# Performance work log

Hardware: AMD Instinct MI355X
Metric: run time of the kernel (lower is better)

## Reference

```python
import jax, jax.numpy as jnp
import numpy as np

NUM_CLASSES = 81
BACKGROUND = 0
TOP_K = 200
KEEP_TOP_K = 200
CONF_THR = 0.01
NMS_THR = 0.45
B = 32
P = 24564  # SSD512 prior count


def setup_inputs() -> dict:
    key = jax.random.key(0)
    k1, k2, kc, ks = jax.random.split(key, 4)
    loc_data = jax.random.normal(k1, (B, P * 4), jnp.float32) * 0.5
    conf_data = jax.random.uniform(k2, (B, P * NUM_CLASSES), dtype=jnp.float32)
    # priors in corner form [xmin,ymin,xmax,ymax] within [0,1], plus Caffe-style variances
    ctr = jax.random.uniform(kc, (P, 2), minval=0.05, maxval=0.95, dtype=jnp.float32)
    sz = jax.random.uniform(ks, (P, 2), minval=0.02, maxval=0.30, dtype=jnp.float32)
    pboxes = jnp.concatenate([ctr - sz * 0.5, ctr + sz * 0.5], axis=1)  # [P,4]
    variances = jnp.tile(jnp.array([0.1, 0.1, 0.2, 0.2], jnp.float32), (P, 1))  # [P,4]
    prior_data = jnp.stack([pboxes, variances], axis=0).reshape(1, 2, P * 4)
    return {"loc_data": loc_data, "conf_data": conf_data, "prior_data": prior_data}


def _decode(loc, priors, variances):
    # CENTER_SIZE decode, Caffe DetectionOutput convention (priors in corner form).
    pw = priors[:, 2] - priors[:, 0]
    ph = priors[:, 3] - priors[:, 1]
    pcx = (priors[:, 0] + priors[:, 2]) * 0.5
    pcy = (priors[:, 1] + priors[:, 3]) * 0.5
    cx = variances[:, 0] * loc[:, 0] * pw + pcx
    cy = variances[:, 1] * loc[:, 1] * ph + pcy
    w = jnp.exp(variances[:, 2] * loc[:, 2]) * pw
    h = jnp.exp(variances[:, 3] * loc[:, 3]) * ph
    return jnp.stack([cx - w * 0.5, cy - h * 0.5, cx + w * 0.5, cy + h * 0.5], axis=-1)


def _pairwise_iou(b):  # [K,4] -> [K,K]
    x1 = jnp.maximum(b[:, None, 0], b[None, :, 0])
    y1 = jnp.maximum(b[:, None, 1], b[None, :, 1])
    x2 = jnp.minimum(b[:, None, 2], b[None, :, 2])
    y2 = jnp.minimum(b[:, None, 3], b[None, :, 3])
    inter = jnp.clip(x2 - x1, 0.0) * jnp.clip(y2 - y1, 0.0)
    area = jnp.clip(b[:, 2] - b[:, 0], 0.0) * jnp.clip(b[:, 3] - b[:, 1], 0.0)
    union = area[:, None] + area[None, :] - inter
    return inter / jnp.maximum(union, 1e-10)


def _nms_one_class(scores, boxes):
    # scores: [P], boxes: [P,4] -> kept scores [TOP_K], candidate boxes [TOP_K,4]
    s = jnp.where(scores > CONF_THR, scores, -1.0)
    vals, idx = jax.lax.top_k(s, TOP_K)
    cand = boxes[idx]                      # [TOP_K,4]
    iou = _pairwise_iou(cand)              # [TOP_K,TOP_K]
    valid = vals > CONF_THR

    def body(i, carry):
        keep, suppressed = carry
        is_kept = valid[i] & jnp.logical_not(suppressed[i])
        keep = keep.at[i].set(is_kept)
        suppressed = suppressed | (is_kept & (iou[i] > NMS_THR))
        return keep, suppressed

    keep, _ = jax.lax.fori_loop(
        0, TOP_K, body,
        (jnp.zeros((TOP_K,), jnp.bool_), jnp.zeros((TOP_K,), jnp.bool_)))
    kept_scores = jnp.where(keep, vals, 0.0)
    return kept_scores, cand


def _detection_output(loc_data, conf_data, prior_data):
    bsz = loc_data.shape[0]
    nprior = loc_data.shape[1] // 4
    loc = loc_data.reshape(bsz, nprior, 4)
    conf = conf_data.reshape(bsz, nprior, NUM_CLASSES).transpose(0, 2, 1)  # [B,C,P]
    pr = prior_data.reshape(2, nprior, 4)
    priors, variances = pr[0], pr[1]

    decoded = jax.vmap(lambda l: _decode(l, priors, variances))(loc)  # [B,P,4]

    # kill background class
    bg = (jnp.arange(NUM_CLASSES) == BACKGROUND)[None, :, None]
    conf = jnp.where(bg, -1.0, conf)

    nms_bc = jax.vmap(jax.vmap(_nms_one_class, in_axes=(0, None)), in_axes=(0, 0))
    scores, cboxes = nms_bc(conf, decoded)  # [B,C,TOP_K], [B,C,TOP_K,4]

    flat_s = scores.reshape(bsz, NUM_CLASSES * TOP_K)
    top_s, top_i = jax.lax.top_k(flat_s, KEEP_TOP_K)          # [B,KEEP]
    labels = (top_i // TOP_K).astype(jnp.float32)
    flat_b = cboxes.reshape(bsz, NUM_CLASSES * TOP_K, 4)
    top_b = jnp.take_along_axis(flat_b, top_i[..., None], axis=1)  # [B,KEEP,4]

    img_id = jnp.broadcast_to(
        jnp.arange(bsz, dtype=jnp.float32)[:, None], (bsz, KEEP_TOP_K))
    rows = jnp.concatenate(
        [img_id[..., None], labels[..., None], top_s[..., None], top_b], axis=-1)
    rows = jnp.where((top_s > 0.0)[..., None], rows, 0.0)
    return rows[:, None, :, :]  # [B,1,KEEP_TOP_K,7]


def reference(loc_data, conf_data, prior_data):
    return _detection_output(loc_data, conf_data, prior_data)
```

## Files before the change

kernel.cpp:

```cpp
#include <hip/hip_runtime.h>
#include <stdint.h>

typedef uint32_t u32;
typedef uint64_t u64;
typedef uint16_t u16;

#define NCLS 81
#define TOPK 200
#define KEEPK 200
#define CONF_THR 0.01f
#define NMS_THR 0.45f
#define NB 32
#define NP 24564
#define NFLAT (NCLS * TOPK)
#define NPCHUNK 256
#define NCHUNK ((NP + NPCHUNK - 1) / NPCHUNK)
#define CAP 512
#define NBC (NB * NCLS)
#define LCAP 16
#define THRF 0.98828125f

__device__ __forceinline__ u32 fkey(float f) {
  u32 u = __float_as_uint(f);
  return (u & 0x80000000u) ? ~u : (u | 0x80000000u);
}
__device__ __forceinline__ float unfkey(u32 k) {
  u32 u = (k & 0x80000000u) ? (k & 0x7FFFFFFFu) : ~k;
  return __uint_as_float(u);
}

__global__ __launch_bounds__(256) void collect_cands(const float* __restrict__ conf,
                                                     u32* __restrict__ lcnt,
                                                     u64* __restrict__ lcand) {
  __shared__ u32 cnt81[NCLS];
  __shared__ u64 stage[NCLS * LCAP];

  const int tid = threadIdx.x;
  const int blk = blockIdx.x;
  const int b = blk / NCHUNK, chunk = blk % NCHUNK;
  const int p0 = chunk * NPCHUNK;
  const int cntp = min(NPCHUNK, NP - p0);
  const int tot4 = (cntp * NCLS) >> 2;
  const float4* __restrict__ src = (const float4*)(conf + ((size_t)b * NP + p0) * NCLS);

  for (int i = tid; i < NCLS; i += 256) cnt81[i] = 0u;
  __syncthreads();

  auto push = [&](int f, float s) {
    u32 pi = (u32)f / (u32)NCLS;
    u32 c = (u32)f - pi * (u32)NCLS;
    if (c != 0u) {
      u32 sl = atomicAdd(&cnt81[c], 1u);
      if (sl < (u32)LCAP) {
        u32 p = (u32)p0 + pi;
        stage[c * LCAP + sl] = ((u64)fkey(s) << 32) | (u32)(~p);
      }
    }
  };
  auto proc = [&](float4 v, int i4) {
    if (v.x >= THRF) push(i4 * 4 + 0, v.x);
    if (v.y >= THRF) push(i4 * 4 + 1, v.y);
    if (v.z >= THRF) push(i4 * 4 + 2, v.z);
    if (v.w >= THRF) push(i4 * 4 + 3, v.w);
  };

  for (int i = tid; i < tot4; i += 512) {
    int i2 = i + 256;
    bool g2 = i2 < tot4;
    float4 v0 = src[i];
    float4 v1;
    if (g2) v1 = src[i2];
    proc(v0, i);
    if (g2) proc(v1, i2);
  }
  __syncthreads();

  u32* gc = lcnt + (size_t)blk * NCLS;
  for (int i = tid; i < NCLS; i += 256) gc[i] = cnt81[i];
  u64* gl = lcand + (size_t)blk * NCLS * LCAP;
  for (int i = tid; i < NCLS * LCAP; i += 256) gl[i] = stage[i];
}

__global__ __launch_bounds__(256) void perclass_v9(
    const float* __restrict__ loc, const float* __restrict__ conf,
    const float* __restrict__ prior, const u32* __restrict__ lcnt,
    const u64* __restrict__ lcand, float* __restrict__ kept,
    float* __restrict__ cbox) {
  __shared__ u64 cand[CAP];
  __shared__ u32 hist[256];
  __shared__ u32 ck[96], sscan[128];
  __shared__ float bx0[TOPK], bx1[TOPK], bx2[TOPK], bx3[TOPK], barea[TOPK], bscore[TOPK];
  __shared__ u32 s_sel, s_rem, s_cnt, s_cnt2, s_flag;

  const int tid = threadIdx.x;
  const int nwg = NB * NCLS;
  int i0 = blockIdx.x;
  int bc = (i0 & 7) * (nwg / 8) + (i0 >> 3);
  const int b = bc / NCLS, c = bc % NCLS;
  const size_t keptBase = (size_t)bc * TOPK;

  if (c == 0) {
    for (int k = tid; k < TOPK; k += 256) {
      kept[keptBase + k] = 0.f;
      float* bp = cbox + (keptBase + k) * 4;
      bp[0] = 0.f; bp[1] = 0.f; bp[2] = 0.f; bp[3] = 0.f;
    }
    return;
  }

  if (tid == 0) s_flag = 0u;
  if (tid < 128) sscan[tid] = 0u;
  __syncthreads();
  if (tid < 96) {
    u32 m = lcnt[(size_t)(b * NCHUNK + tid) * NCLS + c];
    ck[tid] = m;
    sscan[tid] = m;
    if (m > (u32)LCAP) atomicOr(&s_flag, 1u);
  }
  __syncthreads();
  for (int d = 1; d < 128; d <<= 1) {
    u32 add = 0u;
    if (tid < 128 && tid >= d) add = sscan[tid - d];
    __syncthreads();
    if (tid < 128) sscan[tid] += add;
    __syncthreads();
  }
  const u32 n = sscan[95];
  const bool fast = (s_flag == 0u) && n >= (u32)TOPK && n <= (u32)CAP;

  if (fast) {
    cand[tid] = 0ull; cand[tid + 256] = 0ull;
    __syncthreads();
    if (tid < 96) {
      const u64* srcl = lcand + ((size_t)(b * NCHUNK + tid) * NCLS + c) * LCAP;
      u32 o = sscan[tid] - ck[tid];
      u32 m = ck[tid];
      for (u32 j = 0; j < m; ++j) cand[o + j] = srcl[j];
    }
    __syncthreads();
  } else {
    const float* confb = conf + (size_t)b * NP * NCLS + c;
    auto loadscore = [&](int p) -> float {
      float s = confb[(size_t)p * NCLS];
      return (s > CONF_THR) ? s : -1.0f;
    };
    u32 pfx = 0, K = TOPK;
    for (int shift = 24; shift >= 0; shift -= 8) {
      hist[tid] = 0; __syncthreads();
      u32 himask = (shift == 24) ? 0u : (0xFFFFFFFFu << (shift + 8));
      for (int p = tid; p < NP; p += 256) {
        u32 kf = fkey(loadscore(p));
        if ((kf & himask) == pfx) atomicAdd(&hist[(kf >> shift) & 255u], 1u);
      }
      __syncthreads();
      if (tid == 0) {
        u32 rem = K;
        int bin = 255;
        for (; bin > 0; --bin) {
          u32 cv = hist[bin];
          if (cv >= rem) break;
          rem -= cv;
        }
        s_sel = (u32)bin; s_rem = rem;
      }
      __syncthreads();
      pfx |= s_sel << shift; K = s_rem;
    }
    const u32 T = pfx;
    const u32 G = TOPK - K;
    cand[tid] = 0ull; cand[tid + 256] = 0ull;
    if (tid == 0) { s_cnt = 0; s_cnt2 = 0; }
    __syncthreads();
    for (int p = tid; p < NP; p += 256) {
      u32 kf = fkey(loadscore(p));
      if (kf > T) {
        u32 slot = atomicAdd(&s_cnt, 1u);
        cand[slot] = ((u64)kf << 32) | (u32)(~(u32)p);
      } else if (kf == T) {
        u32 t2 = atomicAdd(&s_cnt2, 1u);
        u32 slot = G + t2;
        if (slot < (u32)CAP) cand[slot] = ((u64)kf << 32) | (u32)(~(u32)p);
      }
    }
    __syncthreads();
  }

  for (u32 k = 2; k <= 512; k <<= 1) {
    for (u32 j = k >> 1; j > 0; j >>= 1) {
      u32 l = ((tid & ~(j - 1)) << 1) | (tid & (j - 1));
      u32 m = l + j;
      u64 a = cand[l], bb = cand[m];
      if (((l & k) == 0) ? (a < bb) : (a > bb)) { cand[l] = bb; cand[m] = a; }
      __syncthreads();
    }
  }

  if (tid < TOPK) {
    u64 e = cand[tid];
    float myscore = unfkey((u32)(e >> 32));
    int p = (int)(~(u32)e);
    const float* lp = loc + ((size_t)b * NP + p) * 4;
    const float* pp = prior + (size_t)p * 4;
    const float* vp = prior + (size_t)NP * 4 + (size_t)p * 4;
    float p0 = pp[0], p1 = pp[1], p2 = pp[2], p3 = pp[3];
    float pw = p2 - p0, ph = p3 - p1;
    float pcx = (p0 + p2) * 0.5f, pcy = (p1 + p3) * 0.5f;
    float cx = vp[0] * lp[0] * pw + pcx;
    float cy = vp[1] * lp[1] * ph + pcy;
    float w = expf(vp[2] * lp[2]) * pw;
    float h = expf(vp[3] * lp[3]) * ph;
    float rx0 = cx - w * 0.5f, ry0 = cy - h * 0.5f;
    float rx1 = cx + w * 0.5f, ry1 = cy + h * 0.5f;
    float rarea = fmaxf(rx1 - rx0, 0.f) * fmaxf(ry1 - ry0, 0.f);
    bx0[tid] = rx0; bx1[tid] = ry0; bx2[tid] = rx1; bx3[tid] = ry1;
    barea[tid] = rarea; bscore[tid] = myscore;
    float* bp = cbox + (keptBase + tid) * 4;
    bp[0] = rx0; bp[1] = ry0; bp[2] = rx1; bp[3] = ry1;
  }
  __syncthreads();

  if (tid < 64) {
    const int lane = tid;
    float sx0[4], sy0[4], sx1[4], sy1[4], sar[4], ssc[4];
    int sup[4] = {0, 0, 0, 0};
    int keepm = 0;
#pragma unroll
    for (int s = 0; s < 4; ++s) {
      int cc2 = s * 64 + lane;
      if (cc2 < TOPK) {
        sx0[s] = bx0[cc2]; sy0[s] = bx1[cc2]; sx1[s] = bx2[cc2]; sy1[s] = bx3[cc2];
        sar[s] = barea[cc2]; ssc[s] = bscore[cc2];
      } else {
        sx0[s] = 0.f; sy0[s] = 0.f; sx1[s] = 0.f; sy1[s] = 0.f;
        sar[s] = 0.f; ssc[s] = -1.f;
      }
    }
#pragma unroll
    for (int s = 0; s < 4; ++s) {
      for (int j = 0; j < 64; ++j) {
        float sc_i = __shfl(ssc[s], j);
        int sup_i = __shfl(sup[s], j);
        if (sc_i > CONF_THR && sup_i == 0) {
          if (j == lane) keepm |= 1 << s;
          float a0 = __shfl(sx0[s], j), a1 = __shfl(sy0[s], j);
          float a2 = __shfl(sx1[s], j), a3 = __shfl(sy1[s], j);
          float aa = __shfl(sar[s], j);
#pragma unroll
          for (int s2 = 0; s2 < 4; ++s2) {
            float xx1 = fmaxf(a0, sx0[s2]), yy1 = fmaxf(a1, sy0[s2]);
            float xx2 = fminf(a2, sx1[s2]), yy2 = fminf(a3, sy1[s2]);
            float inter = fmaxf(xx2 - xx1, 0.f) * fmaxf(yy2 - yy1, 0.f);
            float uni = aa + sar[s2] - inter;
            float iou = inter / fmaxf(uni, 1e-10f);
            if (iou > NMS_THR) sup[s2] = 1;
          }
        }
      }
    }
#pragma unroll
    for (int s = 0; s < 4; ++s) {
      int cc2 = s * 64 + lane;
      if (cc2 < TOPK)
        kept[keptBase + cc2] = ((keepm >> s) & 1) ? ssc[s] : 0.f;
    }
  }
}

__global__ __launch_bounds__(256) void perclass_fallback(
    const float* __restrict__ loc, const float* __restrict__ conf,
    const float* __restrict__ prior, float* __restrict__ kept,
    float* __restrict__ cbox) {
  __shared__ u16 skey[NP];
  __shared__ unsigned int hist[256];
  __shared__ u64 keys[256];
  __shared__ float bx0[TOPK], bx1[TOPK], bx2[TOPK], bx3[TOPK];
  __shared__ float barea[TOPK], bscore[TOPK];
  __shared__ unsigned char sup[TOPK], keepf[TOPK];
  __shared__ unsigned int s_sel, s_rem, s_cnt, s_cnt2;

  const int tid = threadIdx.x;
  const int nwg = NB * NCLS;
  int i0 = blockIdx.x;
  int bc = (i0 & 7) * (nwg / 8) + (i0 >> 3);
  const int b = bc / NCLS, c = bc % NCLS;
  const size_t keptBase = (size_t)bc * TOPK;

  if (c == 0) {
    for (int k = tid; k < TOPK; k += 256) {
      kept[keptBase + k] = 0.f;
      float* bp = cbox + (keptBase + k) * 4;
      bp[0] = 0.f; bp[1] = 0.f; bp[2] = 0.f; bp[3] = 0.f;
    }
    return;
  }

  const float* confb = conf + (size_t)b * NP * NCLS + c;
  auto loadscore = [&](int p) -> float {
    float s = confb[(size_t)p * NCLS];
    return (s > CONF_THR) ? s : -1.0f;
  };

  for (int p = tid; p < NP; p += 256)
    skey[p] = (u16)(fkey(loadscore(p)) >> 16);
  __syncthreads();

  auto select_bin = [&](u32 Kin) {
    if (tid == 0) {
      u32 rem = Kin;
      int bin = 255;
      for (; bin > 0; --bin) {
        u32 cnt = hist[bin];
        if (cnt >= rem) break;
        rem -= cnt;
      }
      s_sel = (u32)bin; s_rem = rem;
    }
    __syncthreads();
  };

  const u32 NEGK16 = 0x407Fu;
  u32 K = TOPK;
  hist[tid] = 0; __syncthreads();
  for (int p = tid; p < NP; p += 256) atomicAdd(&hist[skey[p] >> 8], 1u);
  __syncthreads();
  select_bin(K);
  u32 pfx16 = s_sel << 8; K = s_rem;

  hist[tid] = 0; __syncthreads();
  {
    u32 hb = pfx16 >> 8;
    for (int p = tid; p < NP; p += 256) {
      u16 v = skey[p];
      if ((u32)(v >> 8) == hb) atomicAdd(&hist[v & 255], 1u);
    }
  }
  __syncthreads();
  select_bin(K);
  pfx16 |= s_sel; K = s_rem;

  const bool fillMode = (pfx16 == NEGK16);
  u32 T;
  if (!fillMode) {
    u32 pfull = pfx16 << 16;
    hist[tid] = 0; __syncthreads();
    for (int p = tid; p < NP; p += 256) {
      if ((u32)skey[p] == pfx16) {
        u32 kf = fkey(loadscore(p));
        atomicAdd(&hist[(kf >> 8) & 255], 1u);
      }
    }
    __syncthreads();
    select_bin(K);
    pfull |= s_sel << 8; K = s_rem;

    hist[tid] = 0; __syncthreads();
    for (int p = tid; p < NP; p += 256) {
      if ((u32)skey[p] == pfx16) {
        u32 kf = fkey(loadscore(p));
        if ((kf >> 8) == (pfull >> 8)) atomicAdd(&hist[kf & 255], 1u);
      }
    }
    __syncthreads();
    select_bin(K);
    T = pfull | s_sel; K = s_rem;
  } else {
    T = 0x407FFFFFu;
  }

  const u32 G = TOPK - K;
  keys[tid] = 0;
  if (tid == 0) { s_cnt = 0; s_cnt2 = 0; }
  __syncthreads();
  for (int p = tid; p < NP; p += 256) {
    u32 v = skey[p];
    if (v > pfx16) {
      float s = loadscore(p);
      u32 slot = atomicAdd(&s_cnt, 1u);
      keys[slot] = ((u64)fkey(s) << 32) | (u32)(~(u32)p);
    } else if (!fillMode && v == pfx16) {
      float s = loadscore(p);
      u32 kf = fkey(s);
      if (kf > T) {
        u32 slot = atomicAdd(&s_cnt, 1u);
        keys[slot] = ((u64)kf << 32) | (u32)(~(u32)p);
      } else if (kf == T) {
        u32 t2 = atomicAdd(&s_cnt2, 1u);
        u32 slot = G + t2;
        if (slot < 256u) keys[slot] = ((u64)kf << 32) | (u32)(~(u32)p);
      }
    }
  }
  __syncthreads();
  if (fillMode) {
    for (int k = (int)G + tid; k < TOPK; k += 256)
      keys[k] = ((u64)T << 32) | 0xFFFFFFFFull;
  }
  __syncthreads();

  for (u32 kk = 2; kk <= 256; kk <<= 1) {
    for (u32 j = kk >> 1; j > 0; j >>= 1) {
      u32 ixj = (u32)tid ^ j;
      if (ixj > (u32)tid) {
        u64 a = keys[tid], bb = keys[ixj];
        bool asc = (tid & kk) != 0;
        if (asc ? (a > bb) : (a < bb)) { keys[tid] = bb; keys[ixj] = a; }
      }
      __syncthreads();
    }
  }

  if (tid < TOPK) {
    u64 e = keys[tid];
    float s = unfkey((u32)(e >> 32));
    int p = (int)(~(u32)e);
    const float* lp = loc + ((size_t)b * NP + p) * 4;
    const float* pp = prior + (size_t)p * 4;
    const float* vp = prior + (size_t)NP * 4 + (size_t)p * 4;
    float p0 = pp[0], p1 = pp[1], p2 = pp[2], p3 = pp[3];
    float pw = p2 - p0, ph = p3 - p1;
    float pcx = (p0 + p2) * 0.5f, pcy = (p1 + p3) * 0.5f;
    float cx = vp[0] * lp[0] * pw + pcx;
    float cy = vp[1] * lp[1] * ph + pcy;
    float w = expf(vp[2] * lp[2]) * pw;
    float h = expf(vp[3] * lp[3]) * ph;
    float x0 = cx - w * 0.5f, y0 = cy - h * 0.5f;
    float x1 = cx + w * 0.5f, y1 = cy + h * 0.5f;
    bx0[tid] = x0; bx1[tid] = y0; bx2[tid] = x1; bx3[tid] = y1;
    barea[tid] = fmaxf(x1 - x0, 0.f) * fmaxf(y1 - y0, 0.f);
    bscore[tid] = s;
    sup[tid] = 0;
    keepf[tid] = 0;
  }
  __syncthreads();

  for (int i = 0; i < TOPK; ++i) {
    bool kept_i = (bscore[i] > CONF_THR) && (sup[i] == 0);
    __syncthreads();
    if (kept_i) {
      if (tid < TOPK) {
        float xx1 = fmaxf(bx0[i], bx0[tid]);
        float yy1 = fmaxf(bx1[i], bx1[tid]);
        float xx2 = fminf(bx2[i], bx2[tid]);
        float yy2 = fminf(bx3[i], bx3[tid]);
        float inter = fmaxf(xx2 - xx1, 0.f) * fmaxf(yy2 - yy1, 0.f);
        float uni = barea[i] + barea[tid] - inter;
        float iou = inter / fmaxf(uni, 1e-10f);
        if (iou > NMS_THR) sup[tid] = 1;
      }
      if (tid == 0) keepf[i] = 1;
    }
    __syncthreads();
  }

  if (tid < TOPK) {
    kept[keptBase + tid] = keepf[tid] ? bscore[tid] : 0.f;
    float* bp = cbox + (keptBase + tid) * 4;
    bp[0] = bx0[tid]; bp[1] = bx1[tid]; bp[2] = bx2[tid]; bp[3] = bx3[tid];
  }
}

__global__ __launch_bounds__(256) void final_topk(
    const float* __restrict__ kept, const float* __restrict__ cbox,
    float* __restrict__ out) {
  __shared__ u32 histm[4 * 257];
  __shared__ u32 ssuf[256];
  __shared__ u64 keys[256];
  __shared__ u32 s_sel, s_rem, s_cnt, s_cnt2;

  const int tid = threadIdx.x;
  const int b = blockIdx.x;
  const float* sc = kept + (size_t)b * NFLAT;
  const int sub4 = (tid & 3) * 257;

  auto select256s = [&](u32 Kin) {
    __syncthreads();
    u32 cntv = histm[tid] + histm[257 + tid] + histm[514 + tid] + histm[771 + tid];
    ssuf[tid] = cntv;
    __syncthreads();
    for (int d = 1; d < 256; d <<= 1) {
      u32 add = (tid + d < 256) ? ssuf[tid + d] : 0u;
      __syncthreads();
      ssuf[tid] += add;
      __syncthreads();
    }
    u32 s = ssuf[tid], above = s - cntv;
    if (s >= Kin && above < Kin) { s_sel = (u32)tid; s_rem = Kin - above; }
    __syncthreads();
  };

  u32 pfx = 0;
  u32 K = KEEPK;
  for (int shift = 24; shift >= 0; shift -= 8) {
    for (int j = tid; j < 4 * 257; j += 256) histm[j] = 0u;
    __syncthreads();
    u32 himask = (shift == 24) ? 0u : (0xFFFFFFFFu << (shift + 8));
    for (int p = tid; p < NFLAT; p += 256) {
      u32 kf = fkey(sc[p]);
      if ((kf & himask) == pfx) atomicAdd(&histm[sub4 + ((kf >> shift) & 255u)], 1u);
    }
    select256s(K);
    pfx |= s_sel << shift; K = s_rem;
  }

  const bool fill2 = (pfx == fkey(0.0f));
  const u32 G = KEEPK - K;
  keys[tid] = 0;
  if (tid == 0) { s_cnt = 0; s_cnt2 = 0; }
  __syncthreads();
  for (int p = tid; p < NFLAT; p += 256) {
    u32 kf = fkey(sc[p]);
    if (kf > pfx) {
      u32 slot = atomicAdd(&s_cnt, 1u);
      keys[slot] = ((u64)kf << 32) | (u32)(~(u32)p);
    } else if (!fill2 && kf == pfx) {
      u32 t2 = atomicAdd(&s_cnt2, 1u);
      u32 slot = G + t2;
      if (slot < 256u) keys[slot] = ((u64)kf << 32) | (u32)(~(u32)p);
    }
  }
  __syncthreads();
  if (fill2) {
    for (int k = (int)G + tid; k < KEEPK; k += 256)
      keys[k] = ((u64)pfx << 32) | 0xFFFFFFFFull;
  }
  __syncthreads();

  for (u32 kk = 2; kk <= 256; kk <<= 1) {
    for (u32 j = kk >> 1; j > 0; j >>= 1) {
      u32 ixj = (u32)tid ^ j;
      if (ixj > (u32)tid) {
        u64 a = keys[tid], bb = keys[ixj];
        bool asc = (tid & kk) != 0;
        if (asc ? (a > bb) : (a < bb)) { keys[tid] = bb; keys[ixj] = a; }
      }
      __syncthreads();
    }
  }

  if (tid < KEEPK) {
    u64 e = keys[tid];
    float s = unfkey((u32)(e >> 32));
    u32 fi = ~(u32)e;
    float r0 = 0.f, r1 = 0.f, r2 = 0.f, r3 = 0.f, r4 = 0.f, r5 = 0.f, r6 = 0.f;
    if (s > 0.f) {
      r0 = (float)b;
      r1 = (float)(fi / TOPK);
      r2 = s;
      const float* bp = cbox + ((size_t)b * NFLAT + fi) * 4;
      r3 = bp[0]; r4 = bp[1]; r5 = bp[2]; r6 = bp[3];
    }
    float* op = out + ((size_t)b * KEEPK + tid) * 7;
    op[0] = r0; op[1] = r1; op[2] = r2; op[3] = r3;
    op[4] = r4; op[5] = r5; op[6] = r6;
  }
}

extern "C" void kernel_launch(void* const* d_in, const int* in_sizes, int n_in,
                              void* d_out, int out_size, void* d_ws, size_t ws_size,
                              hipStream_t stream) {
  const float* loc = (const float*)d_in[0];
  const float* conf = (const float*)d_in[1];
  const float* prior = (const float*)d_in[2];
  float* out = (float*)d_out;

  float* kept = (float*)d_ws;
  float* cbox = kept + (size_t)NBC * TOPK;
  const size_t baseBytes = (size_t)NBC * TOPK * 5 * sizeof(float);
  const size_t lcntBytes = (size_t)NB * NCHUNK * NCLS * sizeof(u32);
  const size_t lcandBytes = (size_t)NB * NCHUNK * NCLS * LCAP * sizeof(u64);

  if (ws_size >= baseBytes + lcntBytes + lcandBytes) {
    u32* lcnt = (u32*)((char*)d_ws + baseBytes);
    u64* lcand = (u64*)((char*)d_ws + baseBytes + lcntBytes);
    collect_cands<<<dim3(NB * NCHUNK), dim3(256), 0, stream>>>(conf, lcnt, lcand);
    perclass_v9<<<dim3(NBC), dim3(256), 0, stream>>>(loc, conf, prior, lcnt,
                                                     lcand, kept, cbox);
  } else {
    perclass_fallback<<<dim3(NBC), dim3(256), 0, stream>>>(loc, conf, prior,
                                                           kept, cbox);
  }
  final_topk<<<dim3(NB), dim3(256), 0, stream>>>(kept, cbox, out);
}
```

Baseline: 280.3 us.

## Process four batch-class pairs per workgroup, one wavefront each for sort and NMS

The per-class kernel now packs four (batch, class) problems into each 256-thread workgroup. Candidate gather and prefix scans are shared across the block, while the bitonic sort, box decode and NMS each run on one wavefront per problem. Before, a whole block sorted a single candidate list and only one wavefront did NMS while the other three sat idle, so this aims to make use of those idle wavefronts and cut the block count by four. In exchange, each block uses more shared memory, each wavefront does four times the sort work per stage, and the slow fallback path now runs serially per problem inside the block.

```diff
diff --git a/kernel.cpp b/kernel.cpp
--- a/kernel.cpp
+++ b/kernel.cpp
@@ -17,6 +17,7 @@
 #define NCHUNK ((NP + NPCHUNK - 1) / NPCHUNK)
 #define CAP 512
 #define NBC (NB * NCLS)
+#define NGRP (NBC / 4)
 #define LCAP 16
 #define THRF 0.98828125f
 
@@ -81,64 +82,76 @@
   for (int i = tid; i < NCLS * LCAP; i += 256) gl[i] = stage[i];
 }
 
-__global__ __launch_bounds__(256) void perclass_v9(
+__global__ __launch_bounds__(256) void perclass_v10(
     const float* __restrict__ loc, const float* __restrict__ conf,
     const float* __restrict__ prior, const u32* __restrict__ lcnt,
     const u64* __restrict__ lcand, float* __restrict__ kept,
     float* __restrict__ cbox) {
-  __shared__ u64 cand[CAP];
+  __shared__ u64 cand4[4][CAP];
   __shared__ u32 hist[256];
-  __shared__ u32 ck[96], sscan[128];
-  __shared__ float bx0[TOPK], bx1[TOPK], bx2[TOPK], bx3[TOPK], barea[TOPK], bscore[TOPK];
-  __shared__ u32 s_sel, s_rem, s_cnt, s_cnt2, s_flag;
+  __shared__ u32 ck4[4][96], offs4[4][96];
+  __shared__ u32 sscan[256];
+  __shared__ float bx0[4][TOPK], bx1[4][TOPK], bx2[4][TOPK], bx3[4][TOPK];
+  __shared__ float barea4[4][TOPK], bscore4[4][TOPK];
+  __shared__ u32 nv[4], flagv[4];
+  __shared__ u32 s_sel, s_rem, s_cnt, s_cnt2;
 
   const int tid = threadIdx.x;
-  const int nwg = NB * NCLS;
   int i0 = blockIdx.x;
-  int bc = (i0 & 7) * (nwg / 8) + (i0 >> 3);
-  const int b = bc / NCLS, c = bc % NCLS;
-  const size_t keptBase = (size_t)bc * TOPK;
-
-  if (c == 0) {
-    for (int k = tid; k < TOPK; k += 256) {
-      kept[keptBase + k] = 0.f;
-      float* bp = cbox + (keptBase + k) * 4;
-      bp[0] = 0.f; bp[1] = 0.f; bp[2] = 0.f; bp[3] = 0.f;
-    }
-    return;
-  }
-
-  if (tid == 0) s_flag = 0u;
-  if (tid < 128) sscan[tid] = 0u;
-  __syncthreads();
-  if (tid < 96) {
-    u32 m = lcnt[(size_t)(b * NCHUNK + tid) * NCLS + c];
-    ck[tid] = m;
-    sscan[tid] = m;
-    if (m > (u32)LCAP) atomicOr(&s_flag, 1u);
-  }
-  __syncthreads();
-  for (int d = 1; d < 128; d <<= 1) {
-    u32 add = 0u;
-    if (tid < 128 && tid >= d) add = sscan[tid - d];
-    __syncthreads();
-    if (tid < 128) sscan[tid] += add;
-    __syncthreads();
-  }
-  const u32 n = sscan[95];
-  const bool fast = (s_flag == 0u) && n >= (u32)TOPK && n <= (u32)CAP;
-
-  if (fast) {
-    cand[tid] = 0ull; cand[tid + 256] = 0ull;
-    __syncthreads();
-    if (tid < 96) {
-      const u64* srcl = lcand + ((size_t)(b * NCHUNK + tid) * NCLS + c) * LCAP;
-      u32 o = sscan[tid] - ck[tid];
-      u32 m = ck[tid];
-      for (u32 j = 0; j < m; ++j) cand[o + j] = srcl[j];
-    }
-    __syncthreads();
-  } else {
+  int grp = (i0 & 7) * (NGRP / 8) + (i0 >> 3);
+
+  if (tid < 4) flagv[tid] = 0u;
+  __syncthreads();
+
+  for (int t = tid; t < 384; t += 256) {
+    int g = t / 96, chunk = t - g * 96;
+    int bc = 4 * grp + g;
+    int b = bc / NCLS, c = bc - b * NCLS;
+    u32 m = 0u;
+    if (c != 0) m = lcnt[(size_t)(b * NCHUNK + chunk) * NCLS + c];
+    ck4[g][chunk] = m;
+    if (m > (u32)LCAP) atomicOr(&flagv[g], 1u);
+  }
+  __syncthreads();
+
+  for (int r = 0; r < 2; ++r) {
+    int g = r * 2 + (tid >> 7);
+    int ln = tid & 127;
+    sscan[tid] = (ln < 96) ? ck4[g][ln] : 0u;
+    __syncthreads();
+    for (int d = 1; d < 128; d <<= 1) {
+      u32 add = (ln >= d) ? sscan[tid - d] : 0u;
+      __syncthreads();
+      sscan[tid] += add;
+      __syncthreads();
+    }
+    if (ln < 96) offs4[g][ln] = sscan[tid] - ck4[g][ln];
+    if (ln == 95) nv[g] = sscan[tid];
+    __syncthreads();
+  }
+
+  for (int i = tid; i < 4 * CAP; i += 256) ((u64*)cand4)[i] = 0ull;
+  __syncthreads();
+  for (int t = tid; t < 384; t += 256) {
+    int g = t / 96, chunk = t - g * 96;
+    int bc = 4 * grp + g;
+    int b = bc / NCLS, c = bc - b * NCLS;
+    u32 n = nv[g];
+    bool fast = (flagv[g] == 0u) && n >= (u32)TOPK && n <= (u32)CAP && c != 0;
+    if (fast) {
+      const u64* srcl = lcand + ((size_t)(b * NCHUNK + chunk) * NCLS + c) * LCAP;
+      u32 o = offs4[g][chunk], m = ck4[g][chunk];
+      for (u32 j = 0; j < m; ++j) cand4[g][o + j] = srcl[j];
+    }
+  }
+  __syncthreads();
+
+  for (int g = 0; g < 4; ++g) {
+    int bc = 4 * grp + g;
+    int b = bc / NCLS, c = bc - b * NCLS;
+    u32 n = nv[g];
+    bool fast = (flagv[g] == 0u) && n >= (u32)TOPK && n <= (u32)CAP;
+    if (c == 0 || fast) continue;
     const float* confb = conf + (size_t)b * NP * NCLS + c;
     auto loadscore = [&](int p) -> float {
       float s = confb[(size_t)p * NCLS];
@@ -168,100 +181,126 @@
     }
     const u32 T = pfx;
     const u32 G = TOPK - K;
-    cand[tid] = 0ull; cand[tid + 256] = 0ull;
+    cand4[g][tid] = 0ull; cand4[g][tid + 256] = 0ull;
     if (tid == 0) { s_cnt = 0; s_cnt2 = 0; }
     __syncthreads();
     for (int p = tid; p < NP; p += 256) {
       u32 kf = fkey(loadscore(p));
       if (kf > T) {
         u32 slot = atomicAdd(&s_cnt, 1u);
-        cand[slot] = ((u64)kf << 32) | (u32)(~(u32)p);
+        cand4[g][slot] = ((u64)kf << 32) | (u32)(~(u32)p);
       } else if (kf == T) {
         u32 t2 = atomicAdd(&s_cnt2, 1u);
         u32 slot = G + t2;
-        if (slot < (u32)CAP) cand[slot] = ((u64)kf << 32) | (u32)(~(u32)p);
-      }
-    }
-    __syncthreads();
-  }
-
-  for (u32 k = 2; k <= 512; k <<= 1) {
-    for (u32 j = k >> 1; j > 0; j >>= 1) {
-      u32 l = ((tid & ~(j - 1)) << 1) | (tid & (j - 1));
-      u32 m = l + j;
-      u64 a = cand[l], bb = cand[m];
-      if (((l & k) == 0) ? (a < bb) : (a > bb)) { cand[l] = bb; cand[m] = a; }
-      __syncthreads();
-    }
-  }
-
-  if (tid < TOPK) {
-    u64 e = cand[tid];
-    float myscore = unfkey((u32)(e >> 32));
-    int p = (int)(~(u32)e);
-    const float* lp = loc + ((size_t)b * NP + p) * 4;
-    const float* pp = prior + (size_t)p * 4;
-    const float* vp = prior + (size_t)NP * 4 + (size_t)p * 4;
-    float p0 = pp[0], p1 = pp[1], p2 = pp[2], p3 = pp[3];
-    float pw = p2 - p0, ph = p3 - p1;
-    float pcx = (p0 + p2) * 0.5f, pcy = (p1 + p3) * 0.5f;
-    float cx = vp[0] * lp[0] * pw + pcx;
-    float cy = vp[1] * lp[1] * ph + pcy;
-    float w = expf(vp[2] * lp[2]) * pw;
-    float h = expf(vp[3] * lp[3]) * ph;
-    float rx0 = cx - w * 0.5f, ry0 = cy - h * 0.5f;
-    float rx1 = cx + w * 0.5f, ry1 = cy + h * 0.5f;
-    float rarea = fmaxf(rx1 - rx0, 0.f) * fmaxf(ry1 - ry0, 0.f);
-    bx0[tid] = rx0; bx1[tid] = ry0; bx2[tid] = rx1; bx3[tid] = ry1;
-    barea[tid] = rarea; bscore[tid] = myscore;
-    float* bp = cbox + (keptBase + tid) * 4;
-    bp[0] = rx0; bp[1] = ry0; bp[2] = rx1; bp[3] = ry1;
-  }
-  __syncthreads();
-
-  if (tid < 64) {
-    const int lane = tid;
-    float sx0[4], sy0[4], sx1[4], sy1[4], sar[4], ssc[4];
-    int sup[4] = {0, 0, 0, 0};
-    int keepm = 0;
+        if (slot < (u32)CAP) cand4[g][slot] = ((u64)kf << 32) | (u32)(~(u32)p);
+      }
+    }
+    __syncthreads();
+  }
+
+  {
+    const int w = tid >> 6, ln = tid & 63;
+    u64* cd = cand4[w];
+    for (u32 k = 2; k <= 512; k <<= 1) {
+      for (u32 j = k >> 1; j > 0; j >>= 1) {
+        for (int pi = ln; pi < 256; pi += 64) {
+          u32 l = (((u32)pi & ~(j - 1)) << 1) | ((u32)pi & (j - 1));
+          u32 m = l + j;
+          u64 a = cd[l], bb = cd[m];
+          if (((l & k) == 0) ? (a < bb) : (a > bb)) { cd[l] = bb; cd[m] = a; }
+        }
+        __syncthreads();
+      }
+    }
+  }
+
+  {
+    const int w = tid >> 6, ln = tid & 63;
+    int bc = 4 * grp + w;
+    int b = bc / NCLS, c = bc - b * NCLS;
+    size_t keptBase = (size_t)bc * TOPK;
+    if (c == 0) {
+      for (int idx = ln; idx < TOPK; idx += 64) {
+        kept[keptBase + idx] = 0.f;
+        float* bp = cbox + (keptBase + idx) * 4;
+        bp[0] = 0.f; bp[1] = 0.f; bp[2] = 0.f; bp[3] = 0.f;
+      }
+    } else {
+      for (int idx = ln; idx < TOPK; idx += 64) {
+        u64 e = cand4[w][idx];
+        float myscore = unfkey((u32)(e >> 32));
+        int p = (int)(~(u32)e);
+        const float* lp = loc + ((size_t)b * NP + p) * 4;
+        const float* pp = prior + (size_t)p * 4;
+        const float* vp = prior + (size_t)NP * 4 + (size_t)p * 4;
+        float p0 = pp[0], p1 = pp[1], p2 = pp[2], p3 = pp[3];
+        float pw = p2 - p0, ph = p3 - p1;
+        float pcx = (p0 + p2) * 0.5f, pcy = (p1 + p3) * 0.5f;
+        float cx = vp[0] * lp[0] * pw + pcx;
+        float cy = vp[1] * lp[1] * ph + pcy;
+        float ww = expf(vp[2] * lp[2]) * pw;
+        float hh = expf(vp[3] * lp[3]) * ph;
+        float rx0 = cx - ww * 0.5f, ry0 = cy - hh * 0.5f;
+        float rx1 = cx + ww * 0.5f, ry1 = cy + hh * 0.5f;
+        bx0[w][idx] = rx0; bx1[w][idx] = ry0; bx2[w][idx] = rx1; bx3[w][idx] = ry1;
+        barea4[w][idx] = fmaxf(rx1 - rx0, 0.f) * fmaxf(ry1 - ry0, 0.f);
+        bscore4[w][idx] = myscore;
+        float* bp = cbox + (keptBase + idx) * 4;
+        bp[0] = rx0; bp[1] = ry0; bp[2] = rx1; bp[3] = ry1;
+      }
+    }
+  }
+  __syncthreads();
+
+  {
+    const int w = tid >> 6, lane = tid & 63;
+    int bc = 4 * grp + w;
+    int b = bc / NCLS, c = bc - b * NCLS;
+    size_t keptBase = (size_t)bc * TOPK;
+    if (c != 0) {
+      float sx0[4], sy0[4], sx1[4], sy1[4], sar[4], ssc[4];
+      int sup[4] = {0, 0, 0, 0};
+      int keepm = 0;
 #pragma unroll
-    for (int s = 0; s < 4; ++s) {
-      int cc2 = s * 64 + lane;
-      if (cc2 < TOPK) {
-        sx0[s] = bx0[cc2]; sy0[s] = bx1[cc2]; sx1[s] = bx2[cc2]; sy1[s] = bx3[cc2];
-        sar[s] = barea[cc2]; ssc[s] = bscore[cc2];
-      } else {
-        sx0[s] = 0.f; sy0[s] = 0.f; sx1[s] = 0.f; sy1[s] = 0.f;
-        sar[s] = 0.f; ssc[s] = -1.f;
-      }
-    }
+      for (int s = 0; s < 4; ++s) {
+        int cc2 = s * 64 + lane;
+        if (cc2 < TOPK) {
+          sx0[s] = bx0[w][cc2]; sy0[s] = bx1[w][cc2];
+          sx1[s] = bx2[w][cc2]; sy1[s] = bx3[w][cc2];
+          sar[s] = barea4[w][cc2]; ssc[s] = bscore4[w][cc2];
+        } else {
+          sx0[s] = 0.f; sy0[s] = 0.f; sx1[s] = 0.f; sy1[s] = 0.f;
+          sar[s] = 0.f; ssc[s] = -1.f;
+        }
+      }
 #pragma unroll
-    for (int s = 0; s < 4; ++s) {
-      for (int j = 0; j < 64; ++j) {
-        float sc_i = __shfl(ssc[s], j);
-        int sup_i = __shfl(sup[s], j);
-        if (sc_i > CONF_THR && sup_i == 0) {
-          if (j == lane) keepm |= 1 << s;
-          float a0 = __shfl(sx0[s], j), a1 = __shfl(sy0[s], j);
-          float a2 = __shfl(sx1[s], j), a3 = __shfl(sy1[s], j);
-          float aa = __shfl(sar[s], j);
+      for (int s = 0; s < 4; ++s) {
+        for (int j = 0; j < 64; ++j) {
+          float sc_i = __shfl(ssc[s], j);
+          int sup_i = __shfl(sup[s], j);
+          if (sc_i > CONF_THR && sup_i == 0) {
+            if (j == lane) keepm |= 1 << s;
+            float a0 = __shfl(sx0[s], j), a1 = __shfl(sy0[s], j);
+            float a2 = __shfl(sx1[s], j), a3 = __shfl(sy1[s], j);
+            float aa = __shfl(sar[s], j);
 #pragma unroll
-          for (int s2 = 0; s2 < 4; ++s2) {
-            float xx1 = fmaxf(a0, sx0[s2]), yy1 = fmaxf(a1, sy0[s2]);
-            float xx2 = fminf(a2, sx1[s2]), yy2 = fminf(a3, sy1[s2]);
-            float inter = fmaxf(xx2 - xx1, 0.f) * fmaxf(yy2 - yy1, 0.f);
-            float uni = aa + sar[s2] - inter;
-            float iou = inter / fmaxf(uni, 1e-10f);
-            if (iou > NMS_THR) sup[s2] = 1;
+            for (int s2 = 0; s2 < 4; ++s2) {
+              float xx1 = fmaxf(a0, sx0[s2]), yy1 = fmaxf(a1, sy0[s2]);
+              float xx2 = fminf(a2, sx1[s2]), yy2 = fminf(a3, sy1[s2]);
+              float inter = fmaxf(xx2 - xx1, 0.f) * fmaxf(yy2 - yy1, 0.f);
+              float uni = aa + sar[s2] - inter;
+              float iou = inter / fmaxf(uni, 1e-10f);
+              if (iou > NMS_THR) sup[s2] = 1;
+            }
           }
         }
       }
-    }
 #pragma unroll
-    for (int s = 0; s < 4; ++s) {
-      int cc2 = s * 64 + lane;
-      if (cc2 < TOPK)
-        kept[keptBase + cc2] = ((keepm >> s) & 1) ? ssc[s] : 0.f;
+      for (int s = 0; s < 4; ++s) {
+        int cc2 = s * 64 + lane;
+        if (cc2 < TOPK)
+          kept[keptBase + cc2] = ((keepm >> s) & 1) ? ssc[s] : 0.f;
+      }
     }
   }
 }
@@ -573,8 +612,8 @@
     u32* lcnt = (u32*)((char*)d_ws + baseBytes);
     u64* lcand = (u64*)((char*)d_ws + baseBytes + lcntBytes);
     collect_cands<<<dim3(NB * NCHUNK), dim3(256), 0, stream>>>(conf, lcnt, lcand);
-    perclass_v9<<<dim3(NBC), dim3(256), 0, stream>>>(loc, conf, prior, lcnt,
-                                                     lcand, kept, cbox);
+    perclass_v10<<<dim3(NGRP), dim3(256), 0, stream>>>(loc, conf, prior, lcnt,
+                                                       lcand, kept, cbox);
   } else {
     perclass_fallback<<<dim3(NBC), dim3(256), 0, stream>>>(loc, conf, prior,
                                                            kept, cbox);
```

Measured after the change: 284.2 us. No clear change (+1.4%).
